# Kernel optimization log

Hardware: AMD Instinct MI355X
Metric: run time of the kernel (lower is better)

Reference implementation:

```python
import jax, jax.numpy as jnp
import numpy as np

B, V, M, L, D, OUT = 16, 16, 32, 24, 128, 193
VOCAB = {'cond': 5000, 'proc': 2000, 'drug': 600, 'lab_item': 700, 'lab_value': 200, 'inj_item': 400, 'inj_value': 200}


def setup_inputs() -> dict:
    key = jax.random.key(0)
    ks = iter(jax.random.split(key, 48))
    def emb_table(v):
        t = 0.02 * jax.random.normal(next(ks), (v, D), jnp.float32)
        return t.at[0].set(0.0)  # padding_idx = 0
    inp = {}
    inp['tok_cond'] = jax.random.randint(next(ks), (B, V, L), 0, VOCAB['cond'])
    inp['tok_proc'] = jax.random.randint(next(ks), (B, V, L), 0, VOCAB['proc'])
    inp['tok_drug'] = jax.random.randint(next(ks), (B, V, L), 0, VOCAB['drug'])
    inp['tok_lab_item'] = jax.random.randint(next(ks), (B, V, M, L), 0, VOCAB['lab_item'])
    inp['tok_lab_value'] = jax.random.randint(next(ks), (B, V, M, L), 0, VOCAB['lab_value'])
    inp['tok_inj_item'] = jax.random.randint(next(ks), (B, V, M, L), 0, VOCAB['inj_item'])
    inp['tok_inj_value'] = jax.random.randint(next(ks), (B, V, M, L), 0, VOCAB['inj_value'])
    inp['weight'] = jax.random.uniform(next(ks), (B, V, 1), jnp.float32)
    inp['age'] = jax.random.uniform(next(ks), (B, V, 1), jnp.float32)
    for n in ['cond', 'proc', 'drug', 'lab_item', 'lab_value', 'inj_item', 'inj_value']:
        inp['emb_' + n] = emb_table(VOCAB[n])
    def gru_params(nk):
        s = 0.05
        return (s * jax.random.normal(next(ks), (nk, 3 * D, D), jnp.float32),
                s * jax.random.normal(next(ks), (nk, 3 * D, D), jnp.float32),
                jnp.zeros((nk, 3 * D), jnp.float32),
                jnp.zeros((nk, 3 * D), jnp.float32))
    inp['mgru_wih'], inp['mgru_whh'], inp['mgru_bih'], inp['mgru_bhh'] = gru_params(5)
    inp['vgru_wih'], inp['vgru_whh'], inp['vgru_bih'], inp['vgru_bhh'] = gru_params(7)
    inp['info_w'] = 0.05 * jax.random.normal(next(ks), (2, D), jnp.float32)  # Linear(1, D) weights for weight/age
    inp['info_b'] = jnp.zeros((2, D), jnp.float32)
    inp['fc_w'] = 0.05 * jax.random.normal(next(ks), (7 * D, OUT), jnp.float32)
    inp['fc_b'] = jnp.zeros((OUT,), jnp.float32)
    return inp


def _gru(x, wih, whh, bih, bhh):
    # x: [N, T, Din]; torch nn.GRU semantics, gate order (r, z, n), h0 = 0
    n_, t_, _ = x.shape
    d = whh.shape[1]
    xg = jnp.einsum('ntd,gd->ntg', x, wih) + bih  # precompute input gates [N, T, 3D]
    def step(h, xg_t):
        gh = h @ whh.T + bhh
        ir, iz, inn = jnp.split(xg_t, 3, axis=-1)
        hr, hz, hn = jnp.split(gh, 3, axis=-1)
        r = jax.nn.sigmoid(ir + hr)
        z = jax.nn.sigmoid(iz + hz)
        n = jnp.tanh(inn + r * hn)
        h2 = (1.0 - z) * n + z * h
        return h2, h2
    h0 = jnp.zeros((n_, d), x.dtype)
    hT, outs = jax.lax.scan(step, h0, jnp.swapaxes(xg, 0, 1))
    return jnp.swapaxes(outs, 0, 1), hT  # output [N,T,D], hidden [N,D]

_gru_keys = jax.vmap(_gru)  # vmap over the per-feature-key leading axis


def reference(tok_cond, tok_proc, tok_drug, tok_lab_item, tok_lab_value, tok_inj_item, tok_inj_value,
              weight, age, emb_cond, emb_proc, emb_drug, emb_lab_item, emb_lab_value, emb_inj_item,
              emb_inj_value, mgru_wih, mgru_whh, mgru_bih, mgru_bhh, vgru_wih, vgru_whh, vgru_bih,
              vgru_bhh, info_w, info_b, fc_w, fc_b):
    b, v, m, _ = tok_lab_item.shape
    d = emb_cond.shape[1]
    # visit-event features: embedding + sum over code dim (dropout = identity, eval mode)
    e_cond = emb_cond[tok_cond].sum(axis=2)  # [B,V,D]
    e_proc = emb_proc[tok_proc].sum(axis=2)
    e_drug = emb_drug[tok_drug].sum(axis=2)
    # monitor-event pairs: elementwise mul of the two embeddings, sum over code dim
    lab = (emb_lab_item[tok_lab_item] * emb_lab_value[tok_lab_value]).sum(axis=3)  # [B,V,M,D]
    inj = (emb_inj_item[tok_inj_item] * emb_inj_value[tok_inj_value]).sum(axis=3)
    # repeat visit embeddings across the monitor axis (repeat(1, max_monitors, 1))
    rep = lambda e: jnp.broadcast_to(e[:, :, None, :], (b, v, m, d))
    mon_in = jnp.stack([rep(e_cond), rep(e_proc), rep(e_drug), lab, inj], axis=0)
    mon_in = mon_in.reshape(5, b * v, m, d)  # aggregate_tensors with uniform lengths
    # per-key monitor-level GRUs
    mon_out, mon_h = _gru_keys(mon_in, mgru_wih, mgru_whh, mgru_bih, mgru_bhh)
    # split_tensor + extract_and_transpose: take last monitor step per visit -> [5,B,V,D]
    last = mon_out[:, :, -1, :].reshape(5, b, v, d)
    # patient info Linear(1, D) for weight / age
    w_emb = weight * info_w[0] + info_b[0]  # [B,V,D]
    a_emb = age * info_w[1] + info_b[1]
    vis_in = jnp.concatenate([last, jnp.stack([w_emb, a_emb], axis=0)], axis=0)  # [7,B,V,D]
    # per-key visit-level GRUs
    _, vis_h = _gru_keys(vis_in, vgru_wih, vgru_whh, vgru_bih, vgru_bhh)  # [7,B,D]
    patient_emb = jnp.transpose(vis_h, (1, 0, 2)).reshape(b, 7 * d)  # concatenate_patient_embeddings
    logits = jax.nn.relu(patient_emb) @ fc_w + fc_b  # fc_patient: ReLU -> Linear(7D, output_size)
    return logits
```

## Files before the change

kernel.cpp:

```cpp
#include <hip/hip_runtime.h>
#include <stdint.h>

typedef unsigned short u16;
typedef unsigned int u32;

#define B_ 16
#define V_ 16
#define M_ 32
#define L_ 24
#define D_ 128
#define G_ 384
#define N_ 256
#define NM_ 8192
#define OUT_ 193

using bf16x8 = __attribute__((ext_vector_type(8))) __bf16;
using floatx4 = __attribute__((ext_vector_type(4))) float;

__device__ __forceinline__ float bf2f(u16 u) {
  u32 x = ((u32)u) << 16;
  return __builtin_bit_cast(float, x);
}
__device__ __forceinline__ u16 f2bf(float f) {
  u32 u = __builtin_bit_cast(u32, f);
  u = (u + 0x7FFFu + ((u >> 16) & 1u)) >> 16;
  return (u16)u;
}
__device__ __forceinline__ float sigm_(float x) {
  return __builtin_amdgcn_rcpf(1.0f + __expf(-x));
}
__device__ __forceinline__ float tanh_(float x) {
  float e = __expf(2.0f * x);
  return 1.0f - 2.0f * __builtin_amdgcn_rcpf(e + 1.0f);
}
__device__ __forceinline__ floatx4 mfma16(bf16x8 a, bf16x8 b, floatx4 c) {
  return __builtin_amdgcn_mfma_f32_16x16x32_bf16(a, b, c, 0, 0, 0);
}
__device__ __forceinline__ void lds_barrier() {
  asm volatile("s_waitcnt lgkmcnt(0)\n\ts_barrier" ::: "memory");
}

__global__ __launch_bounds__(256) void k_conv_w(
    const float* __restrict__ mwih, const float* __restrict__ vwih,
    const float* __restrict__ mwhh, const float* __restrict__ vwhh,
    u16* __restrict__ wih_hi, u16* __restrict__ wih_lo,
    u16* __restrict__ whh_hi, u16* __restrict__ whh_lo) {
  const int S5 = 5 * G_ * D_, S12 = 12 * G_ * D_;
  int i = blockIdx.x * 256 + threadIdx.x;
  float v;
  u16 *dh, *dl;
  int o;
  if (i < S12) {
    o = i;
    v = (o < S5) ? mwih[o] : vwih[o - S5];
    dh = wih_hi; dl = wih_lo;
  } else {
    o = i - S12;
    v = (o < S5) ? mwhh[o] : vwhh[o - S5];
    dh = whh_hi; dl = whh_lo;
  }
  u16 h = f2bf(v);
  dh[o] = h;
  dl[o] = f2bf(v - bf2f(h));
}

__global__ __launch_bounds__(128) void k_visit_embed(
    const int* __restrict__ tc, const int* __restrict__ tp, const int* __restrict__ td,
    const float* __restrict__ ec, const float* __restrict__ ep, const float* __restrict__ ed,
    const float* __restrict__ wv, const float* __restrict__ av,
    const float* __restrict__ iw, const float* __restrict__ ib,
    u16* __restrict__ ce_hi, u16* __restrict__ ce_lo,
    u16* __restrict__ vx_hi, u16* __restrict__ vx_lo) {
  int n = blockIdx.x, d = threadIdx.x;
  float a0 = 0.f, a1 = 0.f, a2 = 0.f;
#pragma unroll 4
  for (int l = 0; l < L_; l++) {
    a0 += ec[(size_t)tc[n * L_ + l] * D_ + d];
    a1 += ep[(size_t)tp[n * L_ + l] * D_ + d];
    a2 += ed[(size_t)td[n * L_ + l] * D_ + d];
  }
  size_t o0 = (size_t)n * D_ + d;
  u16 h;
  h = f2bf(a0); ce_hi[o0] = h;              ce_lo[o0] = f2bf(a0 - bf2f(h));
  h = f2bf(a1); ce_hi[(size_t)N_ * D_ + o0] = h; ce_lo[(size_t)N_ * D_ + o0] = f2bf(a1 - bf2f(h));
  h = f2bf(a2); ce_hi[(size_t)2 * N_ * D_ + o0] = h; ce_lo[(size_t)2 * N_ * D_ + o0] = f2bf(a2 - bf2f(h));
  float w = wv[n], a = av[n];
  float v1 = w * iw[d] + ib[d];
  float v2 = a * iw[D_ + d] + ib[D_ + d];
  h = f2bf(v1); vx_hi[(size_t)5 * N_ * D_ + o0] = h; vx_lo[(size_t)5 * N_ * D_ + o0] = f2bf(v1 - bf2f(h));
  h = f2bf(v2); vx_hi[(size_t)6 * N_ * D_ + o0] = h; vx_lo[(size_t)6 * N_ * D_ + o0] = f2bf(v2 - bf2f(h));
}

__global__ __launch_bounds__(128) void k_pair_embed(
    const int* __restrict__ tli, const int* __restrict__ tlv,
    const int* __restrict__ tii, const int* __restrict__ tiv,
    const float* __restrict__ eli, const float* __restrict__ elv,
    const float* __restrict__ eii, const float* __restrict__ eiv,
    u16* __restrict__ mx_hi, u16* __restrict__ mx_lo) {
  int r = blockIdx.x, d = threadIdx.x;
  float al = 0.f, ai = 0.f;
#pragma unroll 4
  for (int l = 0; l < L_; l++) {
    al += eli[(size_t)tli[r * L_ + l] * D_ + d] * elv[(size_t)tlv[r * L_ + l] * D_ + d];
    ai += eii[(size_t)tii[r * L_ + l] * D_ + d] * eiv[(size_t)tiv[r * L_ + l] * D_ + d];
  }
  size_t o = (size_t)r * D_ + d;
  u16 h;
  h = f2bf(al); mx_hi[o] = h;                      mx_lo[o] = f2bf(al - bf2f(h));
  h = f2bf(ai); mx_hi[(size_t)NM_ * D_ + o] = h;   mx_lo[(size_t)NM_ * D_ + o] = f2bf(ai - bf2f(h));
}

__global__ __launch_bounds__(256) void k_gemm_xg(
    const u16* __restrict__ A_hi, const u16* __restrict__ A_lo,
    const u16* __restrict__ W_hi,
    const float* __restrict__ bias,
    float* __restrict__ out, int A_ks, int W_ks, int b_ks, int o_ks) {
  int key = blockIdx.z;
  int w = threadIdx.x >> 6, lane = threadIdx.x & 63;
  int mq = lane & 15, q = lane >> 4;
  int row = blockIdx.x * 64 + w * 16;
  int cb = blockIdx.y * 96;

  const u16* Wk = W_hi + (size_t)key * W_ks;
  bf16x8 wf[6][4];
#pragma unroll
  for (int j = 0; j < 6; j++)
#pragma unroll
    for (int kk = 0; kk < 4; kk++)
      wf[j][kk] = *(const bf16x8*)(Wk + (size_t)(cb + j * 16 + mq) * D_ + kk * 32 + q * 8);

  const u16* Ah = A_hi + (size_t)key * A_ks + (size_t)(row + mq) * D_;
  const u16* Al = A_lo + (size_t)key * A_ks + (size_t)(row + mq) * D_;
  bf16x8 ah[4], al[4];
#pragma unroll
  for (int kk = 0; kk < 4; kk++) {
    ah[kk] = *(const bf16x8*)(Ah + kk * 32 + q * 8);
    al[kk] = *(const bf16x8*)(Al + kk * 32 + q * 8);
  }

  floatx4 acc[6];
#pragma unroll
  for (int j = 0; j < 6; j++) {
    float bv = bias[key * b_ks + cb + j * 16 + mq];
    acc[j] = {bv, bv, bv, bv};
  }
#pragma unroll
  for (int j = 0; j < 6; j++)
#pragma unroll
    for (int kk = 0; kk < 4; kk++) {
      acc[j] = mfma16(ah[kk], wf[j][kk], acc[j]);
      acc[j] = mfma16(al[kk], wf[j][kk], acc[j]);
    }

  float* op = out + (size_t)key * o_ks + (size_t)(row + q * 4) * G_ + cb + mq;
#pragma unroll
  for (int j = 0; j < 6; j++)
#pragma unroll
    for (int i = 0; i < 4; i++) op[(size_t)i * G_ + j * 16] = acc[j][i];
}

template <int MODE, int TT>
__global__ __launch_bounds__(256, 1) void k_gru_t(
    int cpk, const float* __restrict__ xg_a, const float* __restrict__ xg_b,
    const u16* __restrict__ whh_all, const float* __restrict__ bhh_all,
    u16* __restrict__ out_hi, u16* __restrict__ out_lo, float* __restrict__ out_f32) {
  int key = blockIdx.x / cpk;
  int chunk = blockIdx.x % cpk;
  int n0 = chunk * 16;
  const u16* whh = whh_all + (size_t)key * (G_ * D_);
  const float* bhh = bhh_all + (size_t)key * G_;

  __shared__ u16 hls[2][2][16 * 128];

  int tid = threadIdx.x;
  int w = tid >> 6, lane = tid & 63, mq = lane & 15, q = lane >> 4;
  int dA = 16 * w + mq;

  bf16x8 bw[6][4];
#pragma unroll
  for (int j = 0; j < 6; j++)
#pragma unroll
    for (int kk = 0; kk < 4; kk++)
      bw[j][kk] = *(const bf16x8*)(whh + (size_t)(16 * w + 64 * j + mq) * D_ + kk * 32 + q * 8);

  floatx4 bias_v[6];
#pragma unroll
  for (int g = 0; g < 3; g++)
#pragma unroll
    for (int ab = 0; ab < 2; ab++) {
      float b = bhh[g * 128 + ab * 64 + dA];
      bias_v[g * 2 + ab] = {b, b, b, b};
    }

  const float* xbase;
  size_t RS, TS;
  if (MODE == 0) {
    if (key < 3) { xbase = xg_a + ((size_t)key * N_ + n0) * G_; RS = G_; TS = 0; }
    else { xbase = xg_b + ((size_t)(key - 3) * NM_ + (size_t)n0 * M_) * G_; RS = (size_t)M_ * G_; TS = G_; }
  } else {
    xbase = xg_a + (size_t)key * N_ * G_; RS = (size_t)16 * G_; TS = G_;
  }
  const float* rowp[4];
#pragma unroll
  for (int i = 0; i < 4; i++) rowp[i] = xbase + (size_t)(q * 4 + i) * RS + dA;

  float xs[4][24];
#pragma unroll
  for (int s = 0; s < 3; s++) {
    int ts = s < TT ? s : TT - 1;
#pragma unroll
    for (int i = 0; i < 4; i++)
#pragma unroll
      for (int g = 0; g < 3; g++)
#pragma unroll
        for (int ab = 0; ab < 2; ab++)
          xs[s][i * 6 + g * 2 + ab] = rowp[i][(size_t)ts * TS + g * 128 + ab * 64];
  }

  float h_old[8];
#pragma unroll
  for (int k = 0; k < 8; k++) h_old[k] = 0.f;

#define GRU_STEP(P)                                                                        \
  {                                                                                        \
    int t = tb + (P);                                                                      \
    {                                                                                      \
      int tpf = t + 3 < TT ? t + 3 : TT - 1;                                               \
      size_t to = (size_t)tpf * TS;                                                        \
      _Pragma("unroll") for (int i = 0; i < 4; i++)                                        \
          _Pragma("unroll") for (int g = 0; g < 3; g++)                                    \
          _Pragma("unroll") for (int ab = 0; ab < 2; ab++)                                 \
              xs[((P) + 3) & 3][i * 6 + g * 2 + ab] = rowp[i][to + g * 128 + ab * 64];     \
    }                                                                                      \
    floatx4 acc[6];                                                                        \
    if (t > 0) {                                                                           \
      const u16* hp0 = &hls[(t - 1) & 1][0][0];                                            \
      const u16* hp1 = &hls[(t - 1) & 1][1][0];                                            \
      bf16x8 ah[4], al[4];                                                                 \
      _Pragma("unroll") for (int kk = 0; kk < 4; kk++) {                                   \
        int off = mq * 128 + (((kk * 4 + q) ^ mq) * 8);                                    \
        ah[kk] = *(const bf16x8*)(hp0 + off);                                              \
        al[kk] = *(const bf16x8*)(hp1 + off);                                              \
      }                                                                                    \
      _Pragma("unroll") for (int j = 0; j < 6; j++) {                                      \
        floatx4 a = mfma16(ah[0], bw[j][0], bias_v[j]);                                    \
        a = mfma16(al[0], bw[j][0], a);                                                    \
        a = mfma16(ah[1], bw[j][1], a);                                                    \
        a = mfma16(al[1], bw[j][1], a);                                                    \
        a = mfma16(ah[2], bw[j][2], a);                                                    \
        a = mfma16(al[2], bw[j][2], a);                                                    \
        a = mfma16(ah[3], bw[j][3], a);                                                    \
        acc[j] = mfma16(al[3], bw[j][3], a);                                               \
      }                                                                                    \
    } else {                                                                               \
      _Pragma("unroll") for (int j = 0; j < 6; j++) acc[j] = bias_v[j];                    \
    }                                                                                      \
    u16* wrh = &hls[t & 1][0][0];                                                          \
    u16* wrl = &hls[t & 1][1][0];                                                          \
    _Pragma("unroll") for (int i = 0; i < 4; i++) {                                        \
      int row = q * 4 + i;                                                                 \
      _Pragma("unroll") for (int ab = 0; ab < 2; ab++) {                                   \
        float ghr = acc[0 + ab][i];                                                        \
        float ghz = acc[2 + ab][i];                                                        \
        float ghn = acc[4 + ab][i];                                                        \
        float xr = xs[P][i * 6 + 0 + ab];                                                  \
        float xz = xs[P][i * 6 + 2 + ab];                                                  \
        float xnn = xs[P][i * 6 + 4 + ab];                                                 \
        float r = sigm_(xr + ghr);                                                         \
        float z = sigm_(xz + ghz);                                                         \
        float nn = tanh_(xnn + r * ghn);                                                   \
        float h2 = (1.0f - z) * nn + z * h_old[i * 2 + ab];                                \
        h_old[i * 2 + ab] = h2;                                                            \
        u32 ub = __builtin_bit_cast(u32, h2);                                              \
        u16 hb = (u16)(ub >> 16);                                                          \
        float rem = h2 - __builtin_bit_cast(float, ub & 0xFFFF0000u);                      \
        u16 lb = f2bf(rem);                                                                \
        int d = dA + ab * 64;                                                              \
        if (t == TT - 1) {                                                                 \
          if (MODE == 0) {                                                                 \
            size_t o = ((size_t)key * N_ + n0 + row) * D_ + d;                             \
            out_hi[o] = hb;                                                                \
            out_lo[o] = lb;                                                                \
          } else {                                                                         \
            out_f32[((size_t)key * 16 + row) * D_ + d] = h2;                               \
          }                                                                                \
        } else {                                                                           \
          int idx = row * 128 + (((d >> 3) ^ row) * 8) + (d & 7);                          \
          wrh[idx] = hb;                                                                   \
          wrl[idx] = lb;                                                                   \
        }                                                                                  \
      }                                                                                    \
    }                                                                                      \
    if (t + 1 < TT) lds_barrier();                                                         \
  }

#pragma unroll 1
  for (int tb = 0; tb < TT; tb += 4) {
    GRU_STEP(0)
    GRU_STEP(1)
    GRU_STEP(2)
    GRU_STEP(3)
  }
#undef GRU_STEP
}

__global__ __launch_bounds__(256) void k_fc(
    const float* __restrict__ vis_h, const float* __restrict__ fc_w,
    const float* __restrict__ fc_b, float* __restrict__ out) {
  int b = blockIdx.x;
  int cg = blockIdx.y;
  int tid = threadIdx.x;
  int j = tid & 15, s = tid >> 4;
  int c = cg * 16 + j;
  bool cv = c < OUT_;

  __shared__ float hbuf[7 * D_];
  __shared__ float red[16][16];
  for (int i = tid; i < 7 * D_; i += 256) {
    float v = vis_h[((size_t)(i >> 7) * 16 + b) * D_ + (i & 127)];
    hbuf[i] = v > 0.f ? v : 0.f;
  }
  __syncthreads();

  float acc = 0.f;
  if (cv) {
    const float* wp = fc_w + (size_t)(s * 56) * OUT_ + c;
#pragma unroll 8
    for (int k = 0; k < 56; k++) acc += hbuf[s * 56 + k] * wp[(size_t)k * OUT_];
  }
  red[s][j] = acc;
  __syncthreads();
  if (s == 0 && cv) {
    float t = 0.f;
#pragma unroll
    for (int m = 0; m < 16; m++) t += red[m][j];
    out[(size_t)b * OUT_ + c] = t + fc_b[c];
  }
}

extern "C" void kernel_launch(void* const* d_in, const int* in_sizes, int n_in,
                              void* d_out, int out_size, void* d_ws, size_t ws_size,
                              hipStream_t stream) {
  (void)in_sizes; (void)n_in; (void)out_size; (void)ws_size;
  const int* tok_cond = (const int*)d_in[0];
  const int* tok_proc = (const int*)d_in[1];
  const int* tok_drug = (const int*)d_in[2];
  const int* tok_lab_item = (const int*)d_in[3];
  const int* tok_lab_value = (const int*)d_in[4];
  const int* tok_inj_item = (const int*)d_in[5];
  const int* tok_inj_value = (const int*)d_in[6];
  const float* weight = (const float*)d_in[7];
  const float* age = (const float*)d_in[8];
  const float* emb_cond = (const float*)d_in[9];
  const float* emb_proc = (const float*)d_in[10];
  const float* emb_drug = (const float*)d_in[11];
  const float* emb_lab_item = (const float*)d_in[12];
  const float* emb_lab_value = (const float*)d_in[13];
  const float* emb_inj_item = (const float*)d_in[14];
  const float* emb_inj_value = (const float*)d_in[15];
  const float* mgru_wih = (const float*)d_in[16];
  const float* mgru_whh = (const float*)d_in[17];
  const float* mgru_bih = (const float*)d_in[18];
  const float* mgru_bhh = (const float*)d_in[19];
  const float* vgru_wih = (const float*)d_in[20];
  const float* vgru_whh = (const float*)d_in[21];
  const float* vgru_bih = (const float*)d_in[22];
  const float* vgru_bhh = (const float*)d_in[23];
  const float* info_w = (const float*)d_in[24];
  const float* info_b = (const float*)d_in[25];
  const float* fc_w = (const float*)d_in[26];
  const float* fc_b = (const float*)d_in[27];

  char* p = (char*)d_ws;
  auto take = [&](size_t bytes) { char* r = p; p += (bytes + 255) & ~(size_t)255; return r; };
  u16* mon_x_hi = (u16*)take((size_t)2 * NM_ * D_ * 2);
  u16* mon_x_lo = (u16*)take((size_t)2 * NM_ * D_ * 2);
  u16* ce_hi = (u16*)take((size_t)3 * N_ * D_ * 2);
  u16* ce_lo = (u16*)take((size_t)3 * N_ * D_ * 2);
  u16* vis_x_hi = (u16*)take((size_t)7 * N_ * D_ * 2);
  u16* vis_x_lo = (u16*)take((size_t)7 * N_ * D_ * 2);
  float* xg_mon = (float*)take((size_t)2 * NM_ * G_ * 4);
  float* xg_c = (float*)take((size_t)3 * N_ * G_ * 4);
  float* xg_v = (float*)take((size_t)7 * N_ * G_ * 4);
  float* vis_h = (float*)take((size_t)7 * 16 * D_ * 4);
  u16* wih_hi = (u16*)take((size_t)12 * G_ * D_ * 2);
  u16* wih_lo = (u16*)take((size_t)12 * G_ * D_ * 2);
  u16* whh_hi = (u16*)take((size_t)12 * G_ * D_ * 2);
  u16* whh_lo = (u16*)take((size_t)12 * G_ * D_ * 2);

  k_conv_w<<<(24 * G_ * D_) / 256, 256, 0, stream>>>(mgru_wih, vgru_wih, mgru_whh, vgru_whh,
                                                     wih_hi, wih_lo, whh_hi, whh_lo);
  k_visit_embed<<<N_, D_, 0, stream>>>(tok_cond, tok_proc, tok_drug, emb_cond, emb_proc, emb_drug,
                                       weight, age, info_w, info_b, ce_hi, ce_lo, vis_x_hi, vis_x_lo);
  k_pair_embed<<<NM_, D_, 0, stream>>>(tok_lab_item, tok_lab_value, tok_inj_item, tok_inj_value,
                                       emb_lab_item, emb_lab_value, emb_inj_item, emb_inj_value,
                                       mon_x_hi, mon_x_lo);
  k_gemm_xg<<<dim3(NM_ / 64, 4, 2), 256, 0, stream>>>(
      mon_x_hi, mon_x_lo, wih_hi + (size_t)3 * G_ * D_,
      mgru_bih + 3 * G_, xg_mon, NM_ * D_, G_ * D_, G_, NM_ * G_);
  k_gemm_xg<<<dim3(N_ / 64, 4, 3), 256, 0, stream>>>(
      ce_hi, ce_lo, wih_hi, mgru_bih, xg_c, N_ * D_, G_ * D_, G_, N_ * G_);
  k_gru_t<0, 32><<<80, 256, 0, stream>>>(16, xg_c, xg_mon, whh_hi, mgru_bhh,
                                         vis_x_hi, vis_x_lo, nullptr);
  k_gemm_xg<<<dim3(N_ / 64, 4, 7), 256, 0, stream>>>(
      vis_x_hi, vis_x_lo, wih_hi + (size_t)5 * G_ * D_,
      vgru_bih, xg_v, N_ * D_, G_ * D_, G_, N_ * G_);
  k_gru_t<1, 16><<<7, 256, 0, stream>>>(1, xg_v, nullptr, whh_hi + (size_t)5 * G_ * D_, vgru_bhh,
                                        nullptr, nullptr, vis_h);
  k_fc<<<dim3(B_, 13), 256, 0, stream>>>(vis_h, fc_w, fc_b, (float*)d_out);
}
```

Baseline: 235.3 us.

## Fuse embedding/conversion kernels and split GRU recurrence across eight waves

Merges the weight conversion, visit-embedding and pair-embedding kernels into one launch with 256-thread blocks. It also drops the unused low-part bf16 weight copies, which cuts conversion stores. The recurrent GRU kernel now uses 512 threads (8 waves), each owning 16 hidden columns instead of 32. This halves per-wave MFMA chain length, register weights and x prefetch per step, shortening the serial critical path at the cost of a larger barrier group.

```diff
diff --git a/kernel.cpp b/kernel.cpp
--- a/kernel.cpp
+++ b/kernel.cpp
@@ -40,74 +40,71 @@
   asm volatile("s_waitcnt lgkmcnt(0)\n\ts_barrier" ::: "memory");
 }
 
-__global__ __launch_bounds__(256) void k_conv_w(
+#define CONVB 4608
+#define VEB 128
+#define PEB 4096
+
+__global__ __launch_bounds__(256) void k_stage1(
+    const int* __restrict__ tc, const int* __restrict__ tp, const int* __restrict__ td,
+    const int* __restrict__ tli, const int* __restrict__ tlv,
+    const int* __restrict__ tii, const int* __restrict__ tiv,
+    const float* __restrict__ ec, const float* __restrict__ ep, const float* __restrict__ ed,
+    const float* __restrict__ eli, const float* __restrict__ elv,
+    const float* __restrict__ eii, const float* __restrict__ eiv,
+    const float* __restrict__ wv, const float* __restrict__ av,
+    const float* __restrict__ iw, const float* __restrict__ ib,
     const float* __restrict__ mwih, const float* __restrict__ vwih,
     const float* __restrict__ mwhh, const float* __restrict__ vwhh,
-    u16* __restrict__ wih_hi, u16* __restrict__ wih_lo,
-    u16* __restrict__ whh_hi, u16* __restrict__ whh_lo) {
-  const int S5 = 5 * G_ * D_, S12 = 12 * G_ * D_;
-  int i = blockIdx.x * 256 + threadIdx.x;
-  float v;
-  u16 *dh, *dl;
-  int o;
-  if (i < S12) {
-    o = i;
-    v = (o < S5) ? mwih[o] : vwih[o - S5];
-    dh = wih_hi; dl = wih_lo;
+    u16* __restrict__ wih_hi, u16* __restrict__ whh_hi,
+    u16* __restrict__ ce_hi, u16* __restrict__ ce_lo,
+    u16* __restrict__ vx_hi, u16* __restrict__ vx_lo,
+    u16* __restrict__ mx_hi, u16* __restrict__ mx_lo) {
+  int blk = blockIdx.x, tid = threadIdx.x;
+  if (blk < CONVB) {
+    const int SW = 12 * G_ * D_, S5 = 5 * G_ * D_;
+    int i = blk * 256 + tid;
+    if (i < SW) {
+      float v = (i < S5) ? mwih[i] : vwih[i - S5];
+      wih_hi[i] = f2bf(v);
+    } else {
+      int o = i - SW;
+      float v = (o < S5) ? mwhh[o] : vwhh[o - S5];
+      whh_hi[o] = f2bf(v);
+    }
+  } else if (blk < CONVB + VEB) {
+    int n = (blk - CONVB) * 2 + (tid >> 7);
+    int d = tid & 127;
+    float a0 = 0.f, a1 = 0.f, a2 = 0.f;
+#pragma unroll 4
+    for (int l = 0; l < L_; l++) {
+      a0 += ec[(size_t)tc[n * L_ + l] * D_ + d];
+      a1 += ep[(size_t)tp[n * L_ + l] * D_ + d];
+      a2 += ed[(size_t)td[n * L_ + l] * D_ + d];
+    }
+    size_t o0 = (size_t)n * D_ + d;
+    u16 h;
+    h = f2bf(a0); ce_hi[o0] = h;                   ce_lo[o0] = f2bf(a0 - bf2f(h));
+    h = f2bf(a1); ce_hi[(size_t)N_ * D_ + o0] = h; ce_lo[(size_t)N_ * D_ + o0] = f2bf(a1 - bf2f(h));
+    h = f2bf(a2); ce_hi[(size_t)2 * N_ * D_ + o0] = h; ce_lo[(size_t)2 * N_ * D_ + o0] = f2bf(a2 - bf2f(h));
+    float wq = wv[n], aq = av[n];
+    float v1 = wq * iw[d] + ib[d];
+    float v2 = aq * iw[D_ + d] + ib[D_ + d];
+    h = f2bf(v1); vx_hi[(size_t)5 * N_ * D_ + o0] = h; vx_lo[(size_t)5 * N_ * D_ + o0] = f2bf(v1 - bf2f(h));
+    h = f2bf(v2); vx_hi[(size_t)6 * N_ * D_ + o0] = h; vx_lo[(size_t)6 * N_ * D_ + o0] = f2bf(v2 - bf2f(h));
   } else {
-    o = i - S12;
-    v = (o < S5) ? mwhh[o] : vwhh[o - S5];
-    dh = whh_hi; dl = whh_lo;
-  }
-  u16 h = f2bf(v);
-  dh[o] = h;
-  dl[o] = f2bf(v - bf2f(h));
-}
-
-__global__ __launch_bounds__(128) void k_visit_embed(
-    const int* __restrict__ tc, const int* __restrict__ tp, const int* __restrict__ td,
-    const float* __restrict__ ec, const float* __restrict__ ep, const float* __restrict__ ed,
-    const float* __restrict__ wv, const float* __restrict__ av,
-    const float* __restrict__ iw, const float* __restrict__ ib,
-    u16* __restrict__ ce_hi, u16* __restrict__ ce_lo,
-    u16* __restrict__ vx_hi, u16* __restrict__ vx_lo) {
-  int n = blockIdx.x, d = threadIdx.x;
-  float a0 = 0.f, a1 = 0.f, a2 = 0.f;
+    int r = (blk - CONVB - VEB) * 2 + (tid >> 7);
+    int d = tid & 127;
+    float al = 0.f, ai = 0.f;
 #pragma unroll 4
-  for (int l = 0; l < L_; l++) {
-    a0 += ec[(size_t)tc[n * L_ + l] * D_ + d];
-    a1 += ep[(size_t)tp[n * L_ + l] * D_ + d];
-    a2 += ed[(size_t)td[n * L_ + l] * D_ + d];
-  }
-  size_t o0 = (size_t)n * D_ + d;
-  u16 h;
-  h = f2bf(a0); ce_hi[o0] = h;              ce_lo[o0] = f2bf(a0 - bf2f(h));
-  h = f2bf(a1); ce_hi[(size_t)N_ * D_ + o0] = h; ce_lo[(size_t)N_ * D_ + o0] = f2bf(a1 - bf2f(h));
-  h = f2bf(a2); ce_hi[(size_t)2 * N_ * D_ + o0] = h; ce_lo[(size_t)2 * N_ * D_ + o0] = f2bf(a2 - bf2f(h));
-  float w = wv[n], a = av[n];
-  float v1 = w * iw[d] + ib[d];
-  float v2 = a * iw[D_ + d] + ib[D_ + d];
-  h = f2bf(v1); vx_hi[(size_t)5 * N_ * D_ + o0] = h; vx_lo[(size_t)5 * N_ * D_ + o0] = f2bf(v1 - bf2f(h));
-  h = f2bf(v2); vx_hi[(size_t)6 * N_ * D_ + o0] = h; vx_lo[(size_t)6 * N_ * D_ + o0] = f2bf(v2 - bf2f(h));
-}
-
-__global__ __launch_bounds__(128) void k_pair_embed(
-    const int* __restrict__ tli, const int* __restrict__ tlv,
-    const int* __restrict__ tii, const int* __restrict__ tiv,
-    const float* __restrict__ eli, const float* __restrict__ elv,
-    const float* __restrict__ eii, const float* __restrict__ eiv,
-    u16* __restrict__ mx_hi, u16* __restrict__ mx_lo) {
-  int r = blockIdx.x, d = threadIdx.x;
-  float al = 0.f, ai = 0.f;
-#pragma unroll 4
-  for (int l = 0; l < L_; l++) {
-    al += eli[(size_t)tli[r * L_ + l] * D_ + d] * elv[(size_t)tlv[r * L_ + l] * D_ + d];
-    ai += eii[(size_t)tii[r * L_ + l] * D_ + d] * eiv[(size_t)tiv[r * L_ + l] * D_ + d];
-  }
-  size_t o = (size_t)r * D_ + d;
-  u16 h;
-  h = f2bf(al); mx_hi[o] = h;                      mx_lo[o] = f2bf(al - bf2f(h));
-  h = f2bf(ai); mx_hi[(size_t)NM_ * D_ + o] = h;   mx_lo[(size_t)NM_ * D_ + o] = f2bf(ai - bf2f(h));
+    for (int l = 0; l < L_; l++) {
+      al += eli[(size_t)tli[r * L_ + l] * D_ + d] * elv[(size_t)tlv[r * L_ + l] * D_ + d];
+      ai += eii[(size_t)tii[r * L_ + l] * D_ + d] * eiv[(size_t)tiv[r * L_ + l] * D_ + d];
+    }
+    size_t o = (size_t)r * D_ + d;
+    u16 h;
+    h = f2bf(al); mx_hi[o] = h;                    mx_lo[o] = f2bf(al - bf2f(h));
+    h = f2bf(ai); mx_hi[(size_t)NM_ * D_ + o] = h; mx_lo[(size_t)NM_ * D_ + o] = f2bf(ai - bf2f(h));
+  }
 }
 
 __global__ __launch_bounds__(256) void k_gemm_xg(
@@ -160,7 +157,7 @@
 }
 
 template <int MODE, int TT>
-__global__ __launch_bounds__(256, 1) void k_gru_t(
+__global__ __launch_bounds__(512, 1) void k_gru8(
     int cpk, const float* __restrict__ xg_a, const float* __restrict__ xg_b,
     const u16* __restrict__ whh_all, const float* __restrict__ bhh_all,
     u16* __restrict__ out_hi, u16* __restrict__ out_lo, float* __restrict__ out_f32) {
@@ -174,23 +171,21 @@
 
   int tid = threadIdx.x;
   int w = tid >> 6, lane = tid & 63, mq = lane & 15, q = lane >> 4;
-  int dA = 16 * w + mq;
-
-  bf16x8 bw[6][4];
-#pragma unroll
-  for (int j = 0; j < 6; j++)
+  int dA = (w << 4) + mq;
+
+  bf16x8 bw[3][4];
+#pragma unroll
+  for (int g = 0; g < 3; g++)
 #pragma unroll
     for (int kk = 0; kk < 4; kk++)
-      bw[j][kk] = *(const bf16x8*)(whh + (size_t)(16 * w + 64 * j + mq) * D_ + kk * 32 + q * 8);
-
-  floatx4 bias_v[6];
-#pragma unroll
-  for (int g = 0; g < 3; g++)
-#pragma unroll
-    for (int ab = 0; ab < 2; ab++) {
-      float b = bhh[g * 128 + ab * 64 + dA];
-      bias_v[g * 2 + ab] = {b, b, b, b};
-    }
+      bw[g][kk] = *(const bf16x8*)(whh + (size_t)(g * 128 + dA) * D_ + kk * 32 + q * 8);
+
+  floatx4 bseed[3];
+#pragma unroll
+  for (int g = 0; g < 3; g++) {
+    float b = bhh[g * 128 + dA];
+    bseed[g] = {b, b, b, b};
+  }
 
   const float* xbase;
   size_t RS, TS;
@@ -204,7 +199,7 @@
 #pragma unroll
   for (int i = 0; i < 4; i++) rowp[i] = xbase + (size_t)(q * 4 + i) * RS + dA;
 
-  float xs[4][24];
+  float xs[4][12];
 #pragma unroll
   for (int s = 0; s < 3; s++) {
     int ts = s < TT ? s : TT - 1;
@@ -212,14 +207,12 @@
     for (int i = 0; i < 4; i++)
 #pragma unroll
       for (int g = 0; g < 3; g++)
-#pragma unroll
-        for (int ab = 0; ab < 2; ab++)
-          xs[s][i * 6 + g * 2 + ab] = rowp[i][(size_t)ts * TS + g * 128 + ab * 64];
-  }
-
-  float h_old[8];
-#pragma unroll
-  for (int k = 0; k < 8; k++) h_old[k] = 0.f;
+        xs[s][i * 3 + g] = rowp[i][(size_t)ts * TS + g * 128];
+  }
+
+  float h_old[4];
+#pragma unroll
+  for (int k = 0; k < 4; k++) h_old[k] = 0.f;
 
 #define GRU_STEP(P)                                                                        \
   {                                                                                        \
@@ -229,10 +222,9 @@
       size_t to = (size_t)tpf * TS;                                                        \
       _Pragma("unroll") for (int i = 0; i < 4; i++)                                        \
           _Pragma("unroll") for (int g = 0; g < 3; g++)                                    \
-          _Pragma("unroll") for (int ab = 0; ab < 2; ab++)                                 \
-              xs[((P) + 3) & 3][i * 6 + g * 2 + ab] = rowp[i][to + g * 128 + ab * 64];     \
+              xs[((P) + 3) & 3][i * 3 + g] = rowp[i][to + g * 128];                        \
     }                                                                                      \
-    floatx4 acc[6];                                                                        \
+    floatx4 acc[3];                                                                        \
     if (t > 0) {                                                                           \
       const u16* hp0 = &hls[(t - 1) & 1][0][0];                                            \
       const u16* hp1 = &hls[(t - 1) & 1][1][0];                                            \
@@ -242,53 +234,44 @@
         ah[kk] = *(const bf16x8*)(hp0 + off);                                              \
         al[kk] = *(const bf16x8*)(hp1 + off);                                              \
       }                                                                                    \
-      _Pragma("unroll") for (int j = 0; j < 6; j++) {                                      \
-        floatx4 a = mfma16(ah[0], bw[j][0], bias_v[j]);                                    \
-        a = mfma16(al[0], bw[j][0], a);                                                    \
-        a = mfma16(ah[1], bw[j][1], a);                                                    \
-        a = mfma16(al[1], bw[j][1], a);                                                    \
-        a = mfma16(ah[2], bw[j][2], a);                                                    \
-        a = mfma16(al[2], bw[j][2], a);                                                    \
-        a = mfma16(ah[3], bw[j][3], a);                                                    \
-        acc[j] = mfma16(al[3], bw[j][3], a);                                               \
+      _Pragma("unroll") for (int g = 0; g < 3; g++) {                                      \
+        floatx4 a = mfma16(ah[0], bw[g][0], bseed[g]);                                     \
+        a = mfma16(al[0], bw[g][0], a);                                                    \
+        a = mfma16(ah[1], bw[g][1], a);                                                    \
+        a = mfma16(al[1], bw[g][1], a);                                                    \
+        a = mfma16(ah[2], bw[g][2], a);                                                    \
+        a = mfma16(al[2], bw[g][2], a);                                                    \
+        a = mfma16(ah[3], bw[g][3], a);                                                    \
+        acc[g] = mfma16(al[3], bw[g][3], a);                                               \
       }                                                                                    \
     } else {                                                                               \
-      _Pragma("unroll") for (int j = 0; j < 6; j++) acc[j] = bias_v[j];                    \
+      _Pragma("unroll") for (int g = 0; g < 3; g++) acc[g] = bseed[g];                     \
     }                                                                                      \
     u16* wrh = &hls[t & 1][0][0];                                                          \
     u16* wrl = &hls[t & 1][1][0];                                                          \
     _Pragma("unroll") for (int i = 0; i < 4; i++) {                                        \
       int row = q * 4 + i;                                                                 \
-      _Pragma("unroll") for (int ab = 0; ab < 2; ab++) {                                   \
-        float ghr = acc[0 + ab][i];                                                        \
-        float ghz = acc[2 + ab][i];                                                        \
-        float ghn = acc[4 + ab][i];                                                        \
-        float xr = xs[P][i * 6 + 0 + ab];                                                  \
-        float xz = xs[P][i * 6 + 2 + ab];                                                  \
-        float xnn = xs[P][i * 6 + 4 + ab];                                                 \
-        float r = sigm_(xr + ghr);                                                         \
-        float z = sigm_(xz + ghz);                                                         \
-        float nn = tanh_(xnn + r * ghn);                                                   \
-        float h2 = (1.0f - z) * nn + z * h_old[i * 2 + ab];                                \
-        h_old[i * 2 + ab] = h2;                                                            \
-        u32 ub = __builtin_bit_cast(u32, h2);                                              \
-        u16 hb = (u16)(ub >> 16);                                                          \
-        float rem = h2 - __builtin_bit_cast(float, ub & 0xFFFF0000u);                      \
-        u16 lb = f2bf(rem);                                                                \
-        int d = dA + ab * 64;                                                              \
-        if (t == TT - 1) {                                                                 \
-          if (MODE == 0) {                                                                 \
-            size_t o = ((size_t)key * N_ + n0 + row) * D_ + d;                             \
-            out_hi[o] = hb;                                                                \
-            out_lo[o] = lb;                                                                \
-          } else {                                                                         \
-            out_f32[((size_t)key * 16 + row) * D_ + d] = h2;                               \
-          }                                                                                \
+      float r = sigm_(xs[P][i * 3 + 0] + acc[0][i]);                                       \
+      float z = sigm_(xs[P][i * 3 + 1] + acc[1][i]);                                       \
+      float nn = tanh_(xs[P][i * 3 + 2] + r * acc[2][i]);                                  \
+      float h2 = (1.0f - z) * nn + z * h_old[i];                                           \
+      h_old[i] = h2;                                                                       \
+      u32 ub = __builtin_bit_cast(u32, h2);                                                \
+      u16 hb = (u16)(ub >> 16);                                                            \
+      float rem = h2 - __builtin_bit_cast(float, ub & 0xFFFF0000u);                        \
+      u16 lb = f2bf(rem);                                                                  \
+      if (t == TT - 1) {                                                                   \
+        if (MODE == 0) {                                                                   \
+          size_t o = ((size_t)key * N_ + n0 + row) * D_ + dA;                              \
+          out_hi[o] = hb;                                                                  \
+          out_lo[o] = lb;                                                                  \
         } else {                                                                           \
-          int idx = row * 128 + (((d >> 3) ^ row) * 8) + (d & 7);                          \
-          wrh[idx] = hb;                                                                   \
-          wrl[idx] = lb;                                                                   \
+          out_f32[((size_t)key * 16 + row) * D_ + dA] = h2;                                \
         }                                                                                  \
+      } else {                                                                             \
+        int idx = row * 128 + (((dA >> 3) ^ row) * 8) + (dA & 7);                          \
+        wrh[idx] = hb;                                                                     \
+        wrl[idx] = lb;                                                                     \
       }                                                                                    \
     }                                                                                      \
     if (t + 1 < TT) lds_barrier();                                                         \
@@ -373,39 +356,35 @@
 
   char* p = (char*)d_ws;
   auto take = [&](size_t bytes) { char* r = p; p += (bytes + 255) & ~(size_t)255; return r; };
-  u16* mon_x_hi = (u16*)take((size_t)2 * NM_ * D_ * 2);
-  u16* mon_x_lo = (u16*)take((size_t)2 * NM_ * D_ * 2);
+  u16* mx_hi = (u16*)take((size_t)2 * NM_ * D_ * 2);
+  u16* mx_lo = (u16*)take((size_t)2 * NM_ * D_ * 2);
   u16* ce_hi = (u16*)take((size_t)3 * N_ * D_ * 2);
   u16* ce_lo = (u16*)take((size_t)3 * N_ * D_ * 2);
-  u16* vis_x_hi = (u16*)take((size_t)7 * N_ * D_ * 2);
-  u16* vis_x_lo = (u16*)take((size_t)7 * N_ * D_ * 2);
+  u16* vx_hi = (u16*)take((size_t)7 * N_ * D_ * 2);
+  u16* vx_lo = (u16*)take((size_t)7 * N_ * D_ * 2);
   float* xg_mon = (float*)take((size_t)2 * NM_ * G_ * 4);
   float* xg_c = (float*)take((size_t)3 * N_ * G_ * 4);
   float* xg_v = (float*)take((size_t)7 * N_ * G_ * 4);
   float* vis_h = (float*)take((size_t)7 * 16 * D_ * 4);
   u16* wih_hi = (u16*)take((size_t)12 * G_ * D_ * 2);
-  u16* wih_lo = (u16*)take((size_t)12 * G_ * D_ * 2);
   u16* whh_hi = (u16*)take((size_t)12 * G_ * D_ * 2);
-  u16* whh_lo = (u16*)take((size_t)12 * G_ * D_ * 2);
-
-  k_conv_w<<<(24 * G_ * D_) / 256, 256, 0, stream>>>(mgru_wih, vgru_wih, mgru_whh, vgru_whh,
-                                                     wih_hi, wih_lo, whh_hi, whh_lo);
-  k_visit_embed<<<N_, D_, 0, stream>>>(tok_cond, tok_proc, tok_drug, emb_cond, emb_proc, emb_drug,
-                                       weight, age, info_w, info_b, ce_hi, ce_lo, vis_x_hi, vis_x_lo);
-  k_pair_embed<<<NM_, D_, 0, stream>>>(tok_lab_item, tok_lab_value, tok_inj_item, tok_inj_value,
-                                       emb_lab_item, emb_lab_value, emb_inj_item, emb_inj_value,
-                                       mon_x_hi, mon_x_lo);
+
+  k_stage1<<<CONVB + VEB + PEB, 256, 0, stream>>>(
+      tok_cond, tok_proc, tok_drug, tok_lab_item, tok_lab_value, tok_inj_item, tok_inj_value,
+      emb_cond, emb_proc, emb_drug, emb_lab_item, emb_lab_value, emb_inj_item, emb_inj_value,
+      weight, age, info_w, info_b, mgru_wih, vgru_wih, mgru_whh, vgru_whh,
+      wih_hi, whh_hi, ce_hi, ce_lo, vx_hi, vx_lo, mx_hi, mx_lo);
   k_gemm_xg<<<dim3(NM_ / 64, 4, 2), 256, 0, stream>>>(
-      mon_x_hi, mon_x_lo, wih_hi + (size_t)3 * G_ * D_,
+      mx_hi, mx_lo, wih_hi + (size_t)3 * G_ * D_,
       mgru_bih + 3 * G_, xg_mon, NM_ * D_, G_ * D_, G_, NM_ * G_);
   k_gemm_xg<<<dim3(N_ / 64, 4, 3), 256, 0, stream>>>(
       ce_hi, ce_lo, wih_hi, mgru_bih, xg_c, N_ * D_, G_ * D_, G_, N_ * G_);
-  k_gru_t<0, 32><<<80, 256, 0, stream>>>(16, xg_c, xg_mon, whh_hi, mgru_bhh,
-                                         vis_x_hi, vis_x_lo, nullptr);
+  k_gru8<0, 32><<<80, 512, 0, stream>>>(16, xg_c, xg_mon, whh_hi, mgru_bhh,
+                                        vx_hi, vx_lo, nullptr);
   k_gemm_xg<<<dim3(N_ / 64, 4, 7), 256, 0, stream>>>(
-      vis_x_hi, vis_x_lo, wih_hi + (size_t)5 * G_ * D_,
+      vx_hi, vx_lo, wih_hi + (size_t)5 * G_ * D_,
       vgru_bih, xg_v, N_ * D_, G_ * D_, G_, N_ * G_);
-  k_gru_t<1, 16><<<7, 256, 0, stream>>>(1, xg_v, nullptr, whh_hi + (size_t)5 * G_ * D_, vgru_bhh,
-                                        nullptr, nullptr, vis_h);
+  k_gru8<1, 16><<<7, 512, 0, stream>>>(1, xg_v, nullptr, whh_hi + (size_t)5 * G_ * D_, vgru_bhh,
+                                       nullptr, nullptr, vis_h);
   k_fc<<<dim3(B_, 13), 256, 0, stream>>>(vis_h, fc_w, fc_b, (float*)d_out);
 }
```

Measured after the change: 222.0 us. 1.06x faster.
